# Performance work log

Measured on AMD Instinct MI355X. Metric: run time of the kernel, lower is better.

## Reference

```python
import jax, jax.numpy as jnp
import numpy as np

B, F, Q = 1, 20908, 1000000

def setup_inputs() -> dict:
    key = jax.random.key(0)
    k1, k2, k3, k4, k5 = jax.random.split(key, 5)
    triangles = jax.random.normal(k1, (B, F, 3, 3), dtype=jnp.float32)
    face_normals = jax.random.normal(k2, (B, F, 3), dtype=jnp.float32)
    points = jax.random.normal(k3, (B, Q, 3), dtype=jnp.float32)
    closest_faces = jax.random.randint(k4, (B, Q), 0, F, dtype=jnp.int32)
    closest_bcs = jax.random.uniform(k5, (B, Q, 3), dtype=jnp.float32)
    return {"triangles": triangles, "face_normals": face_normals,
            "points": points, "closest_faces": closest_faces,
            "closest_bcs": closest_bcs}

def reference(triangles, face_normals, points, closest_faces, closest_bcs):
    # Post-BVH signed-distance computation (BVH query outputs are inputs here).
    bcs = jnp.clip(closest_bcs, 0.0, 1.0)                     # [B,Q,3]
    batch, num_tri = triangles.shape[:2]
    num_pts = points.shape[1]
    # gather closest triangles: flatten batch*face dim, offset per batch row
    idx = closest_faces.astype(jnp.int32) + (jnp.arange(batch, dtype=jnp.int32) * num_tri)[:, None]
    closest_triangles = triangles.reshape(-1, 3, 3)[idx]       # [B,Q,3,3]
    # barycentric interpolation of the three triangle vertices
    closest_points = jnp.einsum('bqvc,bqv->bqc', closest_triangles, bcs)  # [B,Q,3]
    residual = closest_points - points                         # [B,Q,3]
    norm = jnp.linalg.norm(residual, axis=-1, keepdims=True)
    norm = jnp.where(norm == 0, jnp.ones_like(norm), norm)
    residual_norm = residual / norm                            # [B,Q,3]
    # NOTE: original indexes face_normals[:, closest_faces.flatten(), :];
    # this is shape-consistent only for batch==1 (as used in the repo).
    closest_face_normals = face_normals[:, closest_faces.reshape(-1), :]  # [B,Q,3] when B==1
    dot_pr = jnp.sum(residual_norm * closest_face_normals, axis=-1)       # [B,Q]
    sign = jnp.where(dot_pr > 0, -1.0, 1.0).astype(dot_pr.dtype)
    distances = jnp.sqrt(jnp.sum(residual * residual, axis=-1))           # [B,Q]
    signed_distances = sign * distances
    return (signed_distances, residual_norm, closest_points, closest_faces, bcs)
```

## Files before the change

### kernel.cpp

```cpp
#include <hip/hip_runtime.h>

__global__ void SignedDistance_57698590655052_kernel(
    const float* __restrict__ tri,
    const float* __restrict__ fnorm,
    const float* __restrict__ pts,
    const int*   __restrict__ faces,
    const float* __restrict__ bcs_in,
    float* __restrict__ out,
    int Q)
{
    int q = blockIdx.x * blockDim.x + threadIdx.x;
    if (q >= Q) return;

    int face = faces[q];

    float b0 = fminf(fmaxf(bcs_in[3*q + 0], 0.0f), 1.0f);
    float b1 = fminf(fmaxf(bcs_in[3*q + 1], 0.0f), 1.0f);
    float b2 = fminf(fmaxf(bcs_in[3*q + 2], 0.0f), 1.0f);

    const float* t = tri + 9 * face;
    float t00 = t[0], t01 = t[1], t02 = t[2];
    float t10 = t[3], t11 = t[4], t12 = t[5];
    float t20 = t[6], t21 = t[7], t22 = t[8];

    float cp0 = t00 * b0 + t10 * b1 + t20 * b2;
    float cp1 = t01 * b0 + t11 * b1 + t21 * b2;
    float cp2 = t02 * b0 + t12 * b1 + t22 * b2;

    float p0 = pts[3*q + 0];
    float p1 = pts[3*q + 1];
    float p2 = pts[3*q + 2];

    float r0 = cp0 - p0;
    float r1 = cp1 - p1;
    float r2 = cp2 - p2;

    float ss   = r0*r0 + r1*r1 + r2*r2;
    float dist = sqrtf(ss);
    float nrm  = (dist == 0.0f) ? 1.0f : dist;
    float inv  = 1.0f / nrm;

    float rn0 = r0 * inv;
    float rn1 = r1 * inv;
    float rn2 = r2 * inv;

    float n0 = fnorm[3*face + 0];
    float n1 = fnorm[3*face + 1];
    float n2 = fnorm[3*face + 2];

    float dp   = rn0*n0 + rn1*n1 + rn2*n2;
    float sign = (dp > 0.0f) ? -1.0f : 1.0f;

    out[q] = sign * dist;

    float* rn_out = out + (size_t)Q;
    rn_out[3*q + 0] = rn0;
    rn_out[3*q + 1] = rn1;
    rn_out[3*q + 2] = rn2;

    float* cp_out = out + (size_t)4 * Q;
    cp_out[3*q + 0] = cp0;
    cp_out[3*q + 1] = cp1;
    cp_out[3*q + 2] = cp2;

    out[(size_t)7 * Q + q] = (float)face;

    float* bc_out = out + (size_t)8 * Q;
    bc_out[3*q + 0] = b0;
    bc_out[3*q + 1] = b1;
    bc_out[3*q + 2] = b2;
}

extern "C" void kernel_launch(void* const* d_in, const int* in_sizes, int n_in,
                              void* d_out, int out_size, void* d_ws, size_t ws_size,
                              hipStream_t stream) {
    const float* tri    = (const float*)d_in[0];
    const float* fnorm  = (const float*)d_in[1];
    const float* pts    = (const float*)d_in[2];
    const int*   faces  = (const int*)d_in[3];
    const float* bcs    = (const float*)d_in[4];

    int Q = in_sizes[3];

    int block = 256;
    int grid  = (Q + block - 1) / block;
    SignedDistance_57698590655052_kernel<<<grid, block, 0, stream>>>(
        tri, fnorm, pts, faces, bcs, (float*)d_out, Q);
}
```

Baseline: 106.7 us.

## Process four points per thread with 128-bit vector loads and nontemporal stores

Each thread now handles four consecutive query points, loading points, barycentrics and face indices as packed float4/int4 vectors and writing every output array with 16-byte nontemporal stores. This replaces strided scalar accesses to the 3-component arrays with fully coalesced wide transactions, and keeps streaming outputs from polluting cache so the gathered triangle and normal data stay resident. In exchange, each thread carries more live registers and the grid shrinks fourfold, which may reduce latency hiding for the random triangle gathers. The vector loads also assume 16-byte alignment of each input and output sub-array.

```diff
diff --git a/kernel.cpp b/kernel.cpp
--- a/kernel.cpp
+++ b/kernel.cpp
@@ -1,35 +1,31 @@
 #include <hip/hip_runtime.h>
 
-__global__ void SignedDistance_57698590655052_kernel(
-    const float* __restrict__ tri,
-    const float* __restrict__ fnorm,
-    const float* __restrict__ pts,
-    const int*   __restrict__ faces,
-    const float* __restrict__ bcs_in,
-    float* __restrict__ out,
-    int Q)
+
+typedef float  vf4 __attribute__((ext_vector_type(4)));
+typedef int    vi4 __attribute__((ext_vector_type(4)));
+
+__device__ __forceinline__ void ntstore4(float* p, vf4 v) {
+    __builtin_nontemporal_store(v, (vf4*)p);
+}
+
+struct PtOut {
+    float sd, rn0, rn1, rn2, cp0, cp1, cp2, b0, b1, b2, fc;
+};
+
+__device__ __forceinline__ PtOut compute_pt(
+    const float* __restrict__ tri, const float* __restrict__ fnorm,
+    int face, float p0, float p1, float p2,
+    float bb0, float bb1, float bb2)
 {
-    int q = blockIdx.x * blockDim.x + threadIdx.x;
-    if (q >= Q) return;
-
-    int face = faces[q];
-
-    float b0 = fminf(fmaxf(bcs_in[3*q + 0], 0.0f), 1.0f);
-    float b1 = fminf(fmaxf(bcs_in[3*q + 1], 0.0f), 1.0f);
-    float b2 = fminf(fmaxf(bcs_in[3*q + 2], 0.0f), 1.0f);
+    PtOut o;
+    float b0 = fminf(fmaxf(bb0, 0.0f), 1.0f);
+    float b1 = fminf(fmaxf(bb1, 0.0f), 1.0f);
+    float b2 = fminf(fmaxf(bb2, 0.0f), 1.0f);
 
     const float* t = tri + 9 * face;
-    float t00 = t[0], t01 = t[1], t02 = t[2];
-    float t10 = t[3], t11 = t[4], t12 = t[5];
-    float t20 = t[6], t21 = t[7], t22 = t[8];
-
-    float cp0 = t00 * b0 + t10 * b1 + t20 * b2;
-    float cp1 = t01 * b0 + t11 * b1 + t21 * b2;
-    float cp2 = t02 * b0 + t12 * b1 + t22 * b2;
-
-    float p0 = pts[3*q + 0];
-    float p1 = pts[3*q + 1];
-    float p2 = pts[3*q + 2];
+    float cp0 = t[0]*b0 + t[3]*b1 + t[6]*b2;
+    float cp1 = t[1]*b0 + t[4]*b1 + t[7]*b2;
+    float cp2 = t[2]*b0 + t[5]*b1 + t[8]*b2;
 
     float r0 = cp0 - p0;
     float r1 = cp1 - p1;
@@ -40,35 +36,80 @@
     float nrm  = (dist == 0.0f) ? 1.0f : dist;
     float inv  = 1.0f / nrm;
 
-    float rn0 = r0 * inv;
-    float rn1 = r1 * inv;
-    float rn2 = r2 * inv;
+    float rn0 = r0*inv, rn1 = r1*inv, rn2 = r2*inv;
 
-    float n0 = fnorm[3*face + 0];
-    float n1 = fnorm[3*face + 1];
-    float n2 = fnorm[3*face + 2];
-
-    float dp   = rn0*n0 + rn1*n1 + rn2*n2;
+    const float* nn = fnorm + 3 * face;
+    float dp   = rn0*nn[0] + rn1*nn[1] + rn2*nn[2];
     float sign = (dp > 0.0f) ? -1.0f : 1.0f;
 
-    out[q] = sign * dist;
+    o.sd = sign * dist;
+    o.rn0 = rn0; o.rn1 = rn1; o.rn2 = rn2;
+    o.cp0 = cp0; o.cp1 = cp1; o.cp2 = cp2;
+    o.b0 = b0;  o.b1 = b1;  o.b2 = b2;
+    o.fc = (float)face;
+    return o;
+}
 
+__global__ __launch_bounds__(256)
+void SignedDistance_57698590655052_kernel(
+    const float* __restrict__ tri,
+    const float* __restrict__ fnorm,
+    const float* __restrict__ pts,
+    const int*   __restrict__ faces,
+    const float* __restrict__ bcs_in,
+    float* __restrict__ out,
+    int Q)
+{
+    int t  = blockIdx.x * blockDim.x + threadIdx.x;
+    int q0 = t * 4;
+    if (q0 >= Q) return;
+
+    float* sd_out = out;
     float* rn_out = out + (size_t)Q;
-    rn_out[3*q + 0] = rn0;
-    rn_out[3*q + 1] = rn1;
-    rn_out[3*q + 2] = rn2;
+    float* cp_out = out + (size_t)4 * Q;
+    float* fc_out = out + (size_t)7 * Q;
+    float* bc_out = out + (size_t)8 * Q;
 
-    float* cp_out = out + (size_t)4 * Q;
-    cp_out[3*q + 0] = cp0;
-    cp_out[3*q + 1] = cp1;
-    cp_out[3*q + 2] = cp2;
+    if (q0 + 3 < Q) {
+        vf4 pA = *(const vf4*)(pts + 3*q0 + 0);
+        vf4 pB = *(const vf4*)(pts + 3*q0 + 4);
+        vf4 pC = *(const vf4*)(pts + 3*q0 + 8);
+        vf4 bA = *(const vf4*)(bcs_in + 3*q0 + 0);
+        vf4 bB = *(const vf4*)(bcs_in + 3*q0 + 4);
+        vf4 bC = *(const vf4*)(bcs_in + 3*q0 + 8);
+        vi4 f4 = *(const vi4*)(faces + q0);
 
-    out[(size_t)7 * Q + q] = (float)face;
+        PtOut o0 = compute_pt(tri, fnorm, f4.x, pA.x, pA.y, pA.z, bA.x, bA.y, bA.z);
+        PtOut o1 = compute_pt(tri, fnorm, f4.y, pA.w, pB.x, pB.y, bA.w, bB.x, bB.y);
+        PtOut o2 = compute_pt(tri, fnorm, f4.z, pB.z, pB.w, pC.x, bB.z, bB.w, bC.x);
+        PtOut o3 = compute_pt(tri, fnorm, f4.w, pC.y, pC.z, pC.w, bC.y, bC.z, bC.w);
 
-    float* bc_out = out + (size_t)8 * Q;
-    bc_out[3*q + 0] = b0;
-    bc_out[3*q + 1] = b1;
-    bc_out[3*q + 2] = b2;
+        ntstore4(sd_out + q0, (vf4){o0.sd, o1.sd, o2.sd, o3.sd});
+        ntstore4(fc_out + q0, (vf4){o0.fc, o1.fc, o2.fc, o3.fc});
+
+        ntstore4(rn_out + 3*q0 + 0, (vf4){o0.rn0, o0.rn1, o0.rn2, o1.rn0});
+        ntstore4(rn_out + 3*q0 + 4, (vf4){o1.rn1, o1.rn2, o2.rn0, o2.rn1});
+        ntstore4(rn_out + 3*q0 + 8, (vf4){o2.rn2, o3.rn0, o3.rn1, o3.rn2});
+
+        ntstore4(cp_out + 3*q0 + 0, (vf4){o0.cp0, o0.cp1, o0.cp2, o1.cp0});
+        ntstore4(cp_out + 3*q0 + 4, (vf4){o1.cp1, o1.cp2, o2.cp0, o2.cp1});
+        ntstore4(cp_out + 3*q0 + 8, (vf4){o2.cp2, o3.cp0, o3.cp1, o3.cp2});
+
+        ntstore4(bc_out + 3*q0 + 0, (vf4){o0.b0, o0.b1, o0.b2, o1.b0});
+        ntstore4(bc_out + 3*q0 + 4, (vf4){o1.b1, o1.b2, o2.b0, o2.b1});
+        ntstore4(bc_out + 3*q0 + 8, (vf4){o2.b2, o3.b0, o3.b1, o3.b2});
+    } else {
+        for (int q = q0; q < Q; ++q) {
+            PtOut o = compute_pt(tri, fnorm, faces[q],
+                                 pts[3*q+0], pts[3*q+1], pts[3*q+2],
+                                 bcs_in[3*q+0], bcs_in[3*q+1], bcs_in[3*q+2]);
+            sd_out[q] = o.sd;
+            fc_out[q] = o.fc;
+            rn_out[3*q+0] = o.rn0; rn_out[3*q+1] = o.rn1; rn_out[3*q+2] = o.rn2;
+            cp_out[3*q+0] = o.cp0; cp_out[3*q+1] = o.cp1; cp_out[3*q+2] = o.cp2;
+            bc_out[3*q+0] = o.b0;  bc_out[3*q+1] = o.b1;  bc_out[3*q+2] = o.b2;
+        }
+    }
 }
 
 extern "C" void kernel_launch(void* const* d_in, const int* in_sizes, int n_in,
@@ -83,7 +124,8 @@
     int Q = in_sizes[3];
 
     int block = 256;
-    int grid  = (Q + block - 1) / block;
+    int nthreads = (Q + 3) / 4;
+    int grid  = (nthreads + block - 1) / block;
     SignedDistance_57698590655052_kernel<<<grid, block, 0, stream>>>(
         tri, fnorm, pts, faces, bcs, (float*)d_out, Q);
 }
```

Result: slower. 113.0 us (+5.9%).
